# Performance work log

Measured on AMD Instinct MI355X. Metric: run time of the kernel, lower is better.

Reference implementation:

```python
import jax, jax.numpy as jnp
import numpy as np
from jax import lax

B, N, C_PTS = 16, 4096, 64
NPOINT, RADIUS, NSAMPLE = 1024, 0.2, 32
MLP = [64, 64, 128]


def setup_inputs() -> dict:
    key = jax.random.key(0)
    ks = jax.random.split(key, 8)
    inp = {
        "xyz": jax.random.uniform(ks[0], (B, N, 3), jnp.float32),
        "points": jax.random.normal(ks[1], (B, N, C_PTS), jnp.float32),
    }
    cin = C_PTS + 3  # use_xyz=True concatenates centered xyz
    for i, cout in enumerate(MLP):
        inp[f"W{i}"] = jax.random.normal(ks[2 + 2 * i], (cin, cout), jnp.float32) / np.sqrt(cin).astype(np.float32)
        inp[f"b{i}"] = jnp.zeros((cout,), jnp.float32)
        cin = cout
    return inp


def _fps(xyz, npoint):
    # Farthest point sampling (sequential) -> (B, npoint) int32 indices.
    b, n, _ = xyz.shape

    def body(carry, _):
        mind, far = carry  # mind: (B,N) running min sq-dist, far: (B,) current pick
        cen = jnp.take_along_axis(xyz, far[:, None, None], axis=1)  # (B,1,3)
        d = jnp.sum((xyz - cen) ** 2, -1)  # (B,N)
        mind = jnp.minimum(mind, d)
        nxt = jnp.argmax(mind, -1).astype(jnp.int32)
        return (mind, nxt), far

    init = (jnp.full((b, n), 1e10, jnp.float32), jnp.zeros((b,), jnp.int32))
    _, idx = lax.scan(body, init, None, length=npoint)
    return jnp.transpose(idx)  # (B, npoint)


def _ball_query(radius, nsample, xyz, new_xyz):
    # First `nsample` point indices (in original order) within `radius` of each
    # center; short groups padded with the first found index (TF op semantics).
    n = xyz.shape[1]
    d2 = jnp.sum((new_xyz[:, :, None, :] - xyz[:, None, :, :]) ** 2, -1)  # (B,S,N)
    keyv = jnp.where(d2 <= radius * radius, jnp.arange(n, dtype=jnp.int32), n)
    idx = jnp.sort(keyv, axis=-1)[:, :, :nsample]  # smallest indices first
    first = idx[:, :, :1]
    idx = jnp.where(idx == n, first, idx)
    return jnp.minimum(idx, n - 1)


def _group(t, idx):
    # t: (B,N,C), idx: (B,S,K) -> (B,S,K,C)
    return jax.vmap(lambda tb, ib: tb[ib])(t, idx)


def reference(xyz, points, W0, b0, W1, b1, W2, b2):
    fps_idx = _fps(xyz, NPOINT)  # (B,S)
    new_xyz = jnp.take_along_axis(xyz, fps_idx[..., None], axis=1)  # (B,S,3)
    idx = _ball_query(RADIUS, NSAMPLE, xyz, new_xyz)  # (B,S,K)
    grouped_xyz = _group(xyz, idx) - new_xyz[:, :, None, :]  # (B,S,K,3) centered
    grouped_pts = _group(points, idx)  # (B,S,K,C)
    new_points = jnp.concatenate([grouped_xyz, grouped_pts], -1)  # (B,S,K,3+C)
    for W, b in ((W0, b0), (W1, b1), (W2, b2)):  # shared MLP = 1x1 conv + relu
        new_points = jax.nn.relu(jnp.einsum('bskc,cd->bskd', new_points, W) + b)
    new_points = jnp.max(new_points, axis=2)  # max-pool over neighbors -> (B,S,128)
    return new_xyz, new_points, idx
```

## Files before the change

kernel.cpp:

```cpp
#include <hip/hip_runtime.h>

#define NB      16
#define NPTS    4096
#define NPOINT  1024
#define NSAMPLE 32

typedef float v2f __attribute__((ext_vector_type(2)));

__device__ __forceinline__ v2f pk_add(v2f a, v2f b) {
  v2f d;
  asm("v_pk_add_f32 %0, %1, %2" : "=v"(d) : "v"(a), "v"(b));
  return d;
}
__device__ __forceinline__ v2f pk_mul(v2f a, v2f b) {
  v2f d;
  asm("v_pk_mul_f32 %0, %1, %2" : "=v"(d) : "v"(a), "v"(b));
  return d;
}
__device__ __forceinline__ float fnegx(float x) {
  return __int_as_float(__float_as_int(x) ^ 0x80000000);
}

template <int C>
__device__ __forceinline__ int dppi(int v) {
  return __builtin_amdgcn_update_dpp(0, v, C, 0xf, 0xf, true);
}

template <int C>
__device__ __forceinline__ unsigned long long dppmax_u64(unsigned long long k) {
  int lo = dppi<C>((int)(unsigned)k);
  int hi = dppi<C>((int)(k >> 32));
  unsigned long long o = ((unsigned long long)(unsigned)hi << 32) | (unsigned)lo;
  return o > k ? o : k;
}

__device__ __forceinline__ unsigned long long swzmax16_u64(unsigned long long k) {
  int lo = __builtin_amdgcn_ds_swizzle((int)(unsigned)k, 0x401F);
  int hi = __builtin_amdgcn_ds_swizzle((int)(k >> 32), 0x401F);
  unsigned long long o = ((unsigned long long)(unsigned)hi << 32) | (unsigned)lo;
  return o > k ? o : k;
}

union SharedA {
  struct {
    float4 lc4[NPTS];
    float scen[NPOINT * 3];
    unsigned long long part[2][16];
  } f;
  float sw[4096];
};

__global__ __launch_bounds__(512) void fps_p1_kernel(
    const float* __restrict__ xyz, const float* __restrict__ pts,
    const float* __restrict__ W0, float* __restrict__ out_xyz,
    float* __restrict__ P1) {
  __shared__ SharedA sm;
  const int t = threadIdx.x;
  if (blockIdx.x < NB) {
    const int b = blockIdx.x;
    const int lane = t & 63;
    const int wid = t >> 6;
    const float* g = xyz + (size_t)b * NPTS * 3;
    for (int j = t; j < NPTS; j += 512)
      sm.f.lc4[j] = make_float4(g[3 * j], g[3 * j + 1], g[3 * j + 2], 0.0f);
    __syncthreads();
    v2f px2[4], py2[4], pz2[4], mind2[4];
    unsigned nlo[8];
#pragma unroll
    for (int p = 0; p < 4; ++p) {
      const int j0 = t + 512 * (2 * p);
      const float4 a = sm.f.lc4[j0];
      const float4 c = sm.f.lc4[j0 + 512];
      px2[p] = (v2f){a.x, c.x};
      py2[p] = (v2f){a.y, c.y};
      pz2[p] = (v2f){a.z, c.z};
      mind2[p] = (v2f){1e10f, 1e10f};
      nlo[2 * p] = ~(unsigned)j0;
      nlo[2 * p + 1] = ~(unsigned)(j0 + 512);
    }
    float cx, cy, cz;
    {
      const float4 c0 = sm.f.lc4[0];
      cx = c0.x; cy = c0.y; cz = c0.z;
    }
    for (int it = 0; it < NPOINT; ++it) {
      if (t == 0) {
        sm.f.scen[3 * it] = cx; sm.f.scen[3 * it + 1] = cy; sm.f.scen[3 * it + 2] = cz;
      }
      const float ncx = fnegx(cx), ncy = fnegx(cy), ncz = fnegx(cz);
      const v2f ncxx = (v2f){ncx, ncx};
      const v2f ncyy = (v2f){ncy, ncy};
      const v2f nczz = (v2f){ncz, ncz};
#pragma unroll
      for (int p = 0; p < 4; ++p) {
        const v2f dx = pk_add(px2[p], ncxx);
        const v2f dy = pk_add(py2[p], ncyy);
        const v2f dz = pk_add(pz2[p], nczz);
        const v2f xx = pk_mul(dx, dx);
        const v2f yy = pk_mul(dy, dy);
        const v2f zz = pk_mul(dz, dz);
        v2f s = pk_add(xx, yy);
        s = pk_add(s, zz);
        mind2[p].x = fminf(mind2[p].x, s.x);
        mind2[p].y = fminf(mind2[p].y, s.y);
      }
      unsigned long long k[8];
#pragma unroll
      for (int p = 0; p < 4; ++p) {
        k[2 * p] = ((unsigned long long)__float_as_uint(mind2[p].x) << 32) | nlo[2 * p];
        k[2 * p + 1] =
            ((unsigned long long)__float_as_uint(mind2[p].y) << 32) | nlo[2 * p + 1];
      }
#pragma unroll
      for (int s = 4; s; s >>= 1)
#pragma unroll
        for (int i = 0; i < s; ++i) k[i] = k[i] > k[i + s] ? k[i] : k[i + s];
      unsigned long long key = k[0];
      key = dppmax_u64<0xB1>(key);
      key = dppmax_u64<0x4E>(key);
      key = dppmax_u64<0x141>(key);
      key = dppmax_u64<0x140>(key);
      key = swzmax16_u64(key);
      const int buf = it & 1;
      if ((lane & 31) == 0) sm.f.part[buf][wid * 2 + (lane >> 5)] = key;
      __syncthreads();
      unsigned long long rk = sm.f.part[buf][lane & 15];
      rk = dppmax_u64<0xB1>(rk);
      rk = dppmax_u64<0x4E>(rk);
      rk = dppmax_u64<0x141>(rk);
      rk = dppmax_u64<0x140>(rk);
      const unsigned idx = ~(unsigned)rk;
      const float4 c4 = sm.f.lc4[idx];
      cx = c4.x; cy = c4.y; cz = c4.z;
    }
    __syncthreads();
    float* ob = out_xyz + (size_t)b * NPOINT * 3;
    for (int i = t; i < NPOINT * 3; i += 512) ob[i] = sm.f.scen[i];
  } else {
    {
      const float4* w4 = (const float4*)(W0 + 192);
      float4* s4 = (float4*)sm.sw;
#pragma unroll
      for (int m = 0; m < 2; ++m) s4[t + 512 * m] = w4[t + 512 * m];
    }
    __syncthreads();
    const size_t r = (size_t)(blockIdx.x - NB) * 512 + t;
    const float* prow = pts + r * 64;
    float acc[64];
#pragma unroll
    for (int d = 0; d < 64; ++d) acc[d] = 0.0f;
#pragma unroll
    for (int cq = 0; cq < 16; ++cq) {
      const float4 p4 = *(const float4*)(prow + cq * 4);
      const float pv[4] = {p4.x, p4.y, p4.z, p4.w};
#pragma unroll
      for (int u = 0; u < 4; ++u) {
        const int c = cq * 4 + u;
#pragma unroll
        for (int d4 = 0; d4 < 16; ++d4) {
          const float4 w = *(const float4*)(&sm.sw[c * 64 + d4 * 4]);
          acc[d4 * 4 + 0] = fmaf(pv[u], w.x, acc[d4 * 4 + 0]);
          acc[d4 * 4 + 1] = fmaf(pv[u], w.y, acc[d4 * 4 + 1]);
          acc[d4 * 4 + 2] = fmaf(pv[u], w.z, acc[d4 * 4 + 2]);
          acc[d4 * 4 + 3] = fmaf(pv[u], w.w, acc[d4 * 4 + 3]);
        }
      }
    }
    float* o = P1 + r * 64;
#pragma unroll
    for (int d4 = 0; d4 < 16; ++d4)
      *(float4*)(o + d4 * 4) =
          make_float4(acc[d4 * 4], acc[d4 * 4 + 1], acc[d4 * 4 + 2], acc[d4 * 4 + 3]);
  }
}

__global__ __launch_bounds__(256) void ballq_mlp_kernel(
    const float* __restrict__ xyz, const float* __restrict__ new_xyz,
    const float* __restrict__ P1,
    const float* __restrict__ W0, const float* __restrict__ b0,
    const float* __restrict__ W1, const float* __restrict__ b1,
    const float* __restrict__ W2, const float* __restrict__ b2,
    float* __restrict__ out_np, float* __restrict__ out_idx) {
  __shared__ int sidx[8][NSAMPLE];
  const int t = threadIdx.x;
  const int wv = t >> 6, lane = t & 63;
  const int qbase = blockIdx.x * 8;
  const float r2 = (float)(0.2 * 0.2);
  for (int s = 0; s < 2; ++s) {
    const int ql = wv * 2 + s;
    const int q = qbase + ql;
    const int b = q >> 10;
    const float* g = xyz + (size_t)b * NPTS * 3;
    const float nx = new_xyz[(size_t)q * 3];
    const float ny = new_xyz[(size_t)q * 3 + 1];
    const float nz = new_xyz[(size_t)q * 3 + 2];
    int cnt = 0;
    for (int base = 0; base < NPTS; base += 64) {
      const int j = base + lane;
      const float dx = __fsub_rn(g[3 * j], nx);
      const float dy = __fsub_rn(g[3 * j + 1], ny);
      const float dz = __fsub_rn(g[3 * j + 2], nz);
      const float d2 = __fadd_rn(__fadd_rn(__fmul_rn(dx, dx), __fmul_rn(dy, dy)),
                                 __fmul_rn(dz, dz));
      const bool hit = d2 <= r2;
      const unsigned long long m = __ballot(hit);
      const int pos = cnt + __popcll(m & ((1ull << lane) - 1ull));
      if (hit && pos < NSAMPLE) sidx[ql][pos] = j;
      cnt += __popcll(m);
      if (cnt >= NSAMPLE) break;
    }
    const int capped = cnt < NSAMPLE ? cnt : NSAMPLE;
    if (lane < NSAMPLE) {
      const int v = sidx[ql][lane < capped ? lane : 0];
      sidx[ql][lane] = v;
      out_idx[(size_t)q * NSAMPLE + lane] = (float)v;
    }
  }
  __syncthreads();
  const int k = t & 31;
  const int ql = t >> 5;
  const int q = qbase + ql;
  const int b = q >> 10;
  const int idx = sidx[ql][k];
  const float nx = new_xyz[(size_t)q * 3];
  const float ny = new_xyz[(size_t)q * 3 + 1];
  const float nz = new_xyz[(size_t)q * 3 + 2];
  const float* p = xyz + ((size_t)b * NPTS + idx) * 3;
  const float dx = p[0] - nx, dy = p[1] - ny, dz = p[2] - nz;

  float h1[64];
  const float* p1r = P1 + ((size_t)b * NPTS + idx) * 64;
#pragma unroll
  for (int d4 = 0; d4 < 16; ++d4) {
    const float4 pv = *(const float4*)(p1r + d4 * 4);
    const float pe[4] = {pv.x, pv.y, pv.z, pv.w};
#pragma unroll
    for (int u = 0; u < 4; ++u) {
      const int d = d4 * 4 + u;
      const float v = pe[u] + dx * W0[d] + dy * W0[64 + d] + dz * W0[128 + d] + b0[d];
      h1[d] = fmaxf(v, 0.0f);
    }
  }

  float h2[64];
#pragma unroll
  for (int j4 = 0; j4 < 16; ++j4) {
    const float4 bb = *(const float4*)(&b1[j4 * 4]);
    h2[j4 * 4 + 0] = bb.x; h2[j4 * 4 + 1] = bb.y;
    h2[j4 * 4 + 2] = bb.z; h2[j4 * 4 + 3] = bb.w;
  }
#pragma unroll
  for (int c = 0; c < 64; ++c) {
    const float hc = h1[c];
#pragma unroll
    for (int j4 = 0; j4 < 16; ++j4) {
      const float4 w = *(const float4*)(&W1[c * 64 + j4 * 4]);
      h2[j4 * 4 + 0] = fmaf(hc, w.x, h2[j4 * 4 + 0]);
      h2[j4 * 4 + 1] = fmaf(hc, w.y, h2[j4 * 4 + 1]);
      h2[j4 * 4 + 2] = fmaf(hc, w.z, h2[j4 * 4 + 2]);
      h2[j4 * 4 + 3] = fmaf(hc, w.w, h2[j4 * 4 + 3]);
    }
  }
#pragma unroll
  for (int j = 0; j < 64; ++j) h2[j] = fmaxf(h2[j], 0.0f);

  float* outq = out_np + (size_t)q * 128;
  for (int jb = 0; jb < 4; ++jb) {
    float acc[32];
#pragma unroll
    for (int j8 = 0; j8 < 8; ++j8) {
      const float4 bb = *(const float4*)(&b2[jb * 32 + j8 * 4]);
      acc[j8 * 4 + 0] = bb.x; acc[j8 * 4 + 1] = bb.y;
      acc[j8 * 4 + 2] = bb.z; acc[j8 * 4 + 3] = bb.w;
    }
#pragma unroll
    for (int c = 0; c < 64; ++c) {
      const float hc = h2[c];
#pragma unroll
      for (int j8 = 0; j8 < 8; ++j8) {
        const float4 w = *(const float4*)(&W2[c * 128 + jb * 32 + j8 * 4]);
        acc[j8 * 4 + 0] = fmaf(hc, w.x, acc[j8 * 4 + 0]);
        acc[j8 * 4 + 1] = fmaf(hc, w.y, acc[j8 * 4 + 1]);
        acc[j8 * 4 + 2] = fmaf(hc, w.z, acc[j8 * 4 + 2]);
        acc[j8 * 4 + 3] = fmaf(hc, w.w, acc[j8 * 4 + 3]);
      }
    }
#pragma unroll
    for (int j = 0; j < 32; ++j) acc[j] = fmaxf(acc[j], 0.0f);
#pragma unroll
    for (int msk = 16; msk >= 1; msk >>= 1) {
#pragma unroll
      for (int j = 0; j < 32; ++j) acc[j] = fmaxf(acc[j], __shfl_xor(acc[j], msk, 64));
    }
    if (k == 0) {
#pragma unroll
      for (int j8 = 0; j8 < 8; ++j8)
        *(float4*)(outq + jb * 32 + j8 * 4) =
            make_float4(acc[j8 * 4 + 0], acc[j8 * 4 + 1], acc[j8 * 4 + 2], acc[j8 * 4 + 3]);
    }
  }
}

extern "C" void kernel_launch(void* const* d_in, const int* in_sizes, int n_in,
                              void* d_out, int out_size, void* d_ws, size_t ws_size,
                              hipStream_t stream) {
  const float* xyz = (const float*)d_in[0];
  const float* pts = (const float*)d_in[1];
  const float* W0  = (const float*)d_in[2];
  const float* b0  = (const float*)d_in[3];
  const float* W1  = (const float*)d_in[4];
  const float* b1  = (const float*)d_in[5];
  const float* W2  = (const float*)d_in[6];
  const float* b2  = (const float*)d_in[7];

  float* out      = (float*)d_out;
  float* out_xyz  = out;
  float* out_np   = out + 16 * 1024 * 3;
  float* out_idx  = out_np + 16 * 1024 * 128;

  float* P1 = (float*)d_ws;

  fps_p1_kernel<<<NB + 128, 512, 0, stream>>>(xyz, pts, W0, out_xyz, P1);
  ballq_mlp_kernel<<<2048, 256, 0, stream>>>(xyz, out_xyz, P1,
                                             W0, b0, W1, b1, W2, b2,
                                             out_np, out_idx);
}
```

Baseline: 1.006 ms.

## Fuse FPS, projection and ball-query MLP into one cooperative persistent kernel

Merges the two kernels into a single cooperative launch of 256 blocks. Sixteen blocks run farthest-point sampling and publish centroids in chunks of 64 through release flags. The remaining blocks compute the P1 projection, wait on a global counter, then spin on per-chunk flags so ball query and the MLP overlap with the ongoing FPS instead of waiting for it to finish. This removes the serial dependency between sampling and grouping at the cost of spin-wait synchronization, bounded spin loops that could time out and produce wrong results, and a flag memset. It also splits the FPS shared-memory layout into separate x, y and z arrays.

Result: slower. 1.158 ms (+15.1%).

```diff
diff --git a/kernel.cpp b/kernel.cpp
--- a/kernel.cpp
+++ b/kernel.cpp
@@ -4,6 +4,7 @@
 #define NPTS    4096
 #define NPOINT  1024
 #define NSAMPLE 32
+#define NCHUNK  1024
 
 typedef float v2f __attribute__((ext_vector_type(2)));
 
@@ -41,51 +42,57 @@
   return o > k ? o : k;
 }
 
-union SharedA {
+union SharedU {
   struct {
-    float4 lc4[NPTS];
-    float scen[NPOINT * 3];
+    float lx[NPTS], ly[NPTS], lz[NPTS];
     unsigned long long part[2][16];
   } f;
-  float sw[4096];
+  struct {
+    float sw[4096];
+    int sidx[16][NSAMPLE];
+  } c;
+  char pad[82048];
 };
 
-__global__ __launch_bounds__(512) void fps_p1_kernel(
+__global__ __launch_bounds__(512) void mega_kernel(
     const float* __restrict__ xyz, const float* __restrict__ pts,
-    const float* __restrict__ W0, float* __restrict__ out_xyz,
-    float* __restrict__ P1) {
-  __shared__ SharedA sm;
+    const float* __restrict__ W0, const float* __restrict__ b0,
+    const float* __restrict__ W1, const float* __restrict__ b1,
+    const float* __restrict__ W2, const float* __restrict__ b2,
+    float* __restrict__ out_xyz, float* __restrict__ out_np,
+    float* __restrict__ out_idx, float* __restrict__ P1,
+    int* __restrict__ flags, int* __restrict__ p1done) {
+  __shared__ SharedU sm;
   const int t = threadIdx.x;
+  const int wv = t >> 6, lane = t & 63;
+
   if (blockIdx.x < NB) {
     const int b = blockIdx.x;
-    const int lane = t & 63;
-    const int wid = t >> 6;
     const float* g = xyz + (size_t)b * NPTS * 3;
-    for (int j = t; j < NPTS; j += 512)
-      sm.f.lc4[j] = make_float4(g[3 * j], g[3 * j + 1], g[3 * j + 2], 0.0f);
+    for (int j = t; j < NPTS; j += 512) {
+      sm.f.lx[j] = g[3 * j]; sm.f.ly[j] = g[3 * j + 1]; sm.f.lz[j] = g[3 * j + 2];
+    }
     __syncthreads();
     v2f px2[4], py2[4], pz2[4], mind2[4];
     unsigned nlo[8];
 #pragma unroll
     for (int p = 0; p < 4; ++p) {
       const int j0 = t + 512 * (2 * p);
-      const float4 a = sm.f.lc4[j0];
-      const float4 c = sm.f.lc4[j0 + 512];
-      px2[p] = (v2f){a.x, c.x};
-      py2[p] = (v2f){a.y, c.y};
-      pz2[p] = (v2f){a.z, c.z};
+      px2[p] = (v2f){sm.f.lx[j0], sm.f.lx[j0 + 512]};
+      py2[p] = (v2f){sm.f.ly[j0], sm.f.ly[j0 + 512]};
+      pz2[p] = (v2f){sm.f.lz[j0], sm.f.lz[j0 + 512]};
       mind2[p] = (v2f){1e10f, 1e10f};
       nlo[2 * p] = ~(unsigned)j0;
       nlo[2 * p + 1] = ~(unsigned)(j0 + 512);
     }
-    float cx, cy, cz;
-    {
-      const float4 c0 = sm.f.lc4[0];
-      cx = c0.x; cy = c0.y; cz = c0.z;
-    }
+    float cx = sm.f.lx[0], cy = sm.f.ly[0], cz = sm.f.lz[0];
+    float* ob = out_xyz + (size_t)b * NPOINT * 3;
     for (int it = 0; it < NPOINT; ++it) {
       if (t == 0) {
-        sm.f.scen[3 * it] = cx; sm.f.scen[3 * it + 1] = cy; sm.f.scen[3 * it + 2] = cz;
+        ob[3 * it] = cx; ob[3 * it + 1] = cy; ob[3 * it + 2] = cz;
+        if ((it & 63) == 63)
+          __hip_atomic_store(&flags[b * 16 + (it >> 6)], 1, __ATOMIC_RELEASE,
+                             __HIP_MEMORY_SCOPE_AGENT);
       }
       const float ncx = fnegx(cx), ncy = fnegx(cy), ncz = fnegx(cz);
       const v2f ncxx = (v2f){ncx, ncx};
@@ -122,7 +129,7 @@
       key = dppmax_u64<0x140>(key);
       key = swzmax16_u64(key);
       const int buf = it & 1;
-      if ((lane & 31) == 0) sm.f.part[buf][wid * 2 + (lane >> 5)] = key;
+      if ((lane & 31) == 0) sm.f.part[buf][(t >> 6) * 2 + (lane >> 5)] = key;
       __syncthreads();
       unsigned long long rk = sm.f.part[buf][lane & 15];
       rk = dppmax_u64<0xB1>(rk);
@@ -130,173 +137,183 @@
       rk = dppmax_u64<0x141>(rk);
       rk = dppmax_u64<0x140>(rk);
       const unsigned idx = ~(unsigned)rk;
-      const float4 c4 = sm.f.lc4[idx];
-      cx = c4.x; cy = c4.y; cz = c4.z;
-    }
-    __syncthreads();
-    float* ob = out_xyz + (size_t)b * NPOINT * 3;
-    for (int i = t; i < NPOINT * 3; i += 512) ob[i] = sm.f.scen[i];
+      cx = sm.f.lx[idx]; cy = sm.f.ly[idx]; cz = sm.f.lz[idx];
+    }
   } else {
+    const int nb = (int)gridDim.x - NB;
+    const int cb = (int)blockIdx.x - NB;
     {
       const float4* w4 = (const float4*)(W0 + 192);
-      float4* s4 = (float4*)sm.sw;
-#pragma unroll
-      for (int m = 0; m < 2; ++m) s4[t + 512 * m] = w4[t + 512 * m];
+      float4* s4 = (float4*)sm.c.sw;
+      s4[t] = w4[t]; s4[t + 512] = w4[t + 512];
     }
     __syncthreads();
-    const size_t r = (size_t)(blockIdx.x - NB) * 512 + t;
-    const float* prow = pts + r * 64;
-    float acc[64];
-#pragma unroll
-    for (int d = 0; d < 64; ++d) acc[d] = 0.0f;
-#pragma unroll
-    for (int cq = 0; cq < 16; ++cq) {
-      const float4 p4 = *(const float4*)(prow + cq * 4);
-      const float pv[4] = {p4.x, p4.y, p4.z, p4.w};
-#pragma unroll
-      for (int u = 0; u < 4; ++u) {
-        const int c = cq * 4 + u;
-#pragma unroll
-        for (int d4 = 0; d4 < 16; ++d4) {
-          const float4 w = *(const float4*)(&sm.sw[c * 64 + d4 * 4]);
-          acc[d4 * 4 + 0] = fmaf(pv[u], w.x, acc[d4 * 4 + 0]);
-          acc[d4 * 4 + 1] = fmaf(pv[u], w.y, acc[d4 * 4 + 1]);
-          acc[d4 * 4 + 2] = fmaf(pv[u], w.z, acc[d4 * 4 + 2]);
-          acc[d4 * 4 + 3] = fmaf(pv[u], w.w, acc[d4 * 4 + 3]);
-        }
-      }
-    }
-    float* o = P1 + r * 64;
-#pragma unroll
-    for (int d4 = 0; d4 < 16; ++d4)
-      *(float4*)(o + d4 * 4) =
-          make_float4(acc[d4 * 4], acc[d4 * 4 + 1], acc[d4 * 4 + 2], acc[d4 * 4 + 3]);
-  }
-}
-
-__global__ __launch_bounds__(256) void ballq_mlp_kernel(
-    const float* __restrict__ xyz, const float* __restrict__ new_xyz,
-    const float* __restrict__ P1,
-    const float* __restrict__ W0, const float* __restrict__ b0,
-    const float* __restrict__ W1, const float* __restrict__ b1,
-    const float* __restrict__ W2, const float* __restrict__ b2,
-    float* __restrict__ out_np, float* __restrict__ out_idx) {
-  __shared__ int sidx[8][NSAMPLE];
-  const int t = threadIdx.x;
-  const int wv = t >> 6, lane = t & 63;
-  const int qbase = blockIdx.x * 8;
-  const float r2 = (float)(0.2 * 0.2);
-  for (int s = 0; s < 2; ++s) {
-    const int ql = wv * 2 + s;
-    const int q = qbase + ql;
-    const int b = q >> 10;
-    const float* g = xyz + (size_t)b * NPTS * 3;
-    const float nx = new_xyz[(size_t)q * 3];
-    const float ny = new_xyz[(size_t)q * 3 + 1];
-    const float nz = new_xyz[(size_t)q * 3 + 2];
-    int cnt = 0;
-    for (int base = 0; base < NPTS; base += 64) {
-      const int j = base + lane;
-      const float dx = __fsub_rn(g[3 * j], nx);
-      const float dy = __fsub_rn(g[3 * j + 1], ny);
-      const float dz = __fsub_rn(g[3 * j + 2], nz);
-      const float d2 = __fadd_rn(__fadd_rn(__fmul_rn(dx, dx), __fmul_rn(dy, dy)),
-                                 __fmul_rn(dz, dz));
-      const bool hit = d2 <= r2;
-      const unsigned long long m = __ballot(hit);
-      const int pos = cnt + __popcll(m & ((1ull << lane) - 1ull));
-      if (hit && pos < NSAMPLE) sidx[ql][pos] = j;
-      cnt += __popcll(m);
-      if (cnt >= NSAMPLE) break;
-    }
-    const int capped = cnt < NSAMPLE ? cnt : NSAMPLE;
-    if (lane < NSAMPLE) {
-      const int v = sidx[ql][lane < capped ? lane : 0];
-      sidx[ql][lane] = v;
-      out_idx[(size_t)q * NSAMPLE + lane] = (float)v;
-    }
-  }
-  __syncthreads();
-  const int k = t & 31;
-  const int ql = t >> 5;
-  const int q = qbase + ql;
-  const int b = q >> 10;
-  const int idx = sidx[ql][k];
-  const float nx = new_xyz[(size_t)q * 3];
-  const float ny = new_xyz[(size_t)q * 3 + 1];
-  const float nz = new_xyz[(size_t)q * 3 + 2];
-  const float* p = xyz + ((size_t)b * NPTS + idx) * 3;
-  const float dx = p[0] - nx, dy = p[1] - ny, dz = p[2] - nz;
-
-  float h1[64];
-  const float* p1r = P1 + ((size_t)b * NPTS + idx) * 64;
-#pragma unroll
-  for (int d4 = 0; d4 < 16; ++d4) {
-    const float4 pv = *(const float4*)(p1r + d4 * 4);
-    const float pe[4] = {pv.x, pv.y, pv.z, pv.w};
-#pragma unroll
-    for (int u = 0; u < 4; ++u) {
-      const int d = d4 * 4 + u;
-      const float v = pe[u] + dx * W0[d] + dy * W0[64 + d] + dz * W0[128 + d] + b0[d];
-      h1[d] = fmaxf(v, 0.0f);
-    }
-  }
-
-  float h2[64];
-#pragma unroll
-  for (int j4 = 0; j4 < 16; ++j4) {
-    const float4 bb = *(const float4*)(&b1[j4 * 4]);
-    h2[j4 * 4 + 0] = bb.x; h2[j4 * 4 + 1] = bb.y;
-    h2[j4 * 4 + 2] = bb.z; h2[j4 * 4 + 3] = bb.w;
-  }
-#pragma unroll
-  for (int c = 0; c < 64; ++c) {
-    const float hc = h1[c];
-#pragma unroll
-    for (int j4 = 0; j4 < 16; ++j4) {
-      const float4 w = *(const float4*)(&W1[c * 64 + j4 * 4]);
-      h2[j4 * 4 + 0] = fmaf(hc, w.x, h2[j4 * 4 + 0]);
-      h2[j4 * 4 + 1] = fmaf(hc, w.y, h2[j4 * 4 + 1]);
-      h2[j4 * 4 + 2] = fmaf(hc, w.z, h2[j4 * 4 + 2]);
-      h2[j4 * 4 + 3] = fmaf(hc, w.w, h2[j4 * 4 + 3]);
-    }
-  }
-#pragma unroll
-  for (int j = 0; j < 64; ++j) h2[j] = fmaxf(h2[j], 0.0f);
-
-  float* outq = out_np + (size_t)q * 128;
-  for (int jb = 0; jb < 4; ++jb) {
-    float acc[32];
-#pragma unroll
-    for (int j8 = 0; j8 < 8; ++j8) {
-      const float4 bb = *(const float4*)(&b2[jb * 32 + j8 * 4]);
-      acc[j8 * 4 + 0] = bb.x; acc[j8 * 4 + 1] = bb.y;
-      acc[j8 * 4 + 2] = bb.z; acc[j8 * 4 + 3] = bb.w;
-    }
-#pragma unroll
-    for (int c = 0; c < 64; ++c) {
-      const float hc = h2[c];
-#pragma unroll
-      for (int j8 = 0; j8 < 8; ++j8) {
-        const float4 w = *(const float4*)(&W2[c * 128 + jb * 32 + j8 * 4]);
-        acc[j8 * 4 + 0] = fmaf(hc, w.x, acc[j8 * 4 + 0]);
-        acc[j8 * 4 + 1] = fmaf(hc, w.y, acc[j8 * 4 + 1]);
-        acc[j8 * 4 + 2] = fmaf(hc, w.z, acc[j8 * 4 + 2]);
-        acc[j8 * 4 + 3] = fmaf(hc, w.w, acc[j8 * 4 + 3]);
-      }
-    }
-#pragma unroll
-    for (int j = 0; j < 32; ++j) acc[j] = fmaxf(acc[j], 0.0f);
-#pragma unroll
-    for (int msk = 16; msk >= 1; msk >>= 1) {
-#pragma unroll
-      for (int j = 0; j < 32; ++j) acc[j] = fmaxf(acc[j], __shfl_xor(acc[j], msk, 64));
-    }
-    if (k == 0) {
-#pragma unroll
-      for (int j8 = 0; j8 < 8; ++j8)
-        *(float4*)(outq + jb * 32 + j8 * 4) =
-            make_float4(acc[j8 * 4 + 0], acc[j8 * 4 + 1], acc[j8 * 4 + 2], acc[j8 * 4 + 3]);
+    const int rows_per = (NPTS * NB + nb - 1) / nb;
+    const int r0 = cb * rows_per;
+    const int r1 = min(r0 + rows_per, NPTS * NB);
+    for (int r = r0 + t; r < r1; r += 512) {
+      const float* prow = pts + (size_t)r * 64;
+      float acc[64];
+#pragma unroll
+      for (int d = 0; d < 64; ++d) acc[d] = 0.0f;
+#pragma unroll
+      for (int cq = 0; cq < 16; ++cq) {
+        const float4 p4 = *(const float4*)(prow + cq * 4);
+        const float pv[4] = {p4.x, p4.y, p4.z, p4.w};
+#pragma unroll
+        for (int u = 0; u < 4; ++u) {
+          const int cc = cq * 4 + u;
+#pragma unroll
+          for (int d4 = 0; d4 < 16; ++d4) {
+            const float4 w = *(const float4*)(&sm.c.sw[cc * 64 + d4 * 4]);
+            acc[d4 * 4 + 0] = fmaf(pv[u], w.x, acc[d4 * 4 + 0]);
+            acc[d4 * 4 + 1] = fmaf(pv[u], w.y, acc[d4 * 4 + 1]);
+            acc[d4 * 4 + 2] = fmaf(pv[u], w.z, acc[d4 * 4 + 2]);
+            acc[d4 * 4 + 3] = fmaf(pv[u], w.w, acc[d4 * 4 + 3]);
+          }
+        }
+      }
+      float* o = P1 + (size_t)r * 64;
+#pragma unroll
+      for (int d4 = 0; d4 < 16; ++d4)
+        *(float4*)(o + d4 * 4) = make_float4(acc[d4 * 4 + 0], acc[d4 * 4 + 1],
+                                             acc[d4 * 4 + 2], acc[d4 * 4 + 3]);
+    }
+    __syncthreads();
+    if (t == 0) {
+      __threadfence();
+      __hip_atomic_fetch_add(p1done, 1, __ATOMIC_ACQ_REL, __HIP_MEMORY_SCOPE_AGENT);
+    }
+    {
+      int spins = 0;
+      while (__hip_atomic_load(p1done, __ATOMIC_ACQUIRE, __HIP_MEMORY_SCOPE_AGENT) < nb &&
+             ++spins < (1 << 20))
+        __builtin_amdgcn_s_sleep(2);
+    }
+    const float r2 = (float)(0.2 * 0.2);
+    for (int c = cb; c < NCHUNK; c += nb) {
+      const int s16 = c >> 4, b = c & 15;
+      const int q0 = b * NPOINT + s16 * 16;
+      {
+        int spins = 0;
+        while (__hip_atomic_load(&flags[b * 16 + (s16 >> 2)], __ATOMIC_ACQUIRE,
+                                 __HIP_MEMORY_SCOPE_AGENT) == 0 &&
+               ++spins < (1 << 20))
+          __builtin_amdgcn_s_sleep(2);
+      }
+      const float* g = xyz + (size_t)b * NPTS * 3;
+      for (int s = 0; s < 2; ++s) {
+        const int ql = wv * 2 + s;
+        const int q = q0 + ql;
+        const float nx = out_xyz[(size_t)q * 3];
+        const float ny = out_xyz[(size_t)q * 3 + 1];
+        const float nz = out_xyz[(size_t)q * 3 + 2];
+        int cnt = 0;
+        for (int base = 0; base < NPTS; base += 64) {
+          const int j = base + lane;
+          const float dx = __fsub_rn(g[3 * j], nx);
+          const float dy = __fsub_rn(g[3 * j + 1], ny);
+          const float dz = __fsub_rn(g[3 * j + 2], nz);
+          const float d2 = __fadd_rn(__fadd_rn(__fmul_rn(dx, dx), __fmul_rn(dy, dy)),
+                                     __fmul_rn(dz, dz));
+          const bool hit = d2 <= r2;
+          const unsigned long long m = __ballot(hit);
+          const int pos = cnt + __popcll(m & ((1ull << lane) - 1ull));
+          if (hit && pos < NSAMPLE) sm.c.sidx[ql][pos] = j;
+          cnt += __popcll(m);
+          if (cnt >= NSAMPLE) break;
+        }
+        const int capped = cnt < NSAMPLE ? cnt : NSAMPLE;
+        if (lane < NSAMPLE) {
+          const int v = sm.c.sidx[ql][lane < capped ? lane : 0];
+          sm.c.sidx[ql][lane] = v;
+          out_idx[(size_t)q * NSAMPLE + lane] = (float)v;
+        }
+      }
+      __syncthreads();
+      const int k = t & 31;
+      const int ql = t >> 5;
+      const int q = q0 + ql;
+      const int idx = sm.c.sidx[ql][k];
+      const float nx = out_xyz[(size_t)q * 3];
+      const float ny = out_xyz[(size_t)q * 3 + 1];
+      const float nz = out_xyz[(size_t)q * 3 + 2];
+      const float* p = g + (size_t)idx * 3;
+      const float dx = p[0] - nx, dy = p[1] - ny, dz = p[2] - nz;
+
+      float h1[64];
+      const float* p1r = P1 + ((size_t)b * NPTS + idx) * 64;
+#pragma unroll
+      for (int d4 = 0; d4 < 16; ++d4) {
+        const float4 pv = *(const float4*)(p1r + d4 * 4);
+        const float pe[4] = {pv.x, pv.y, pv.z, pv.w};
+#pragma unroll
+        for (int u = 0; u < 4; ++u) {
+          const int d = d4 * 4 + u;
+          const float v = pe[u] + dx * W0[d] + dy * W0[64 + d] + dz * W0[128 + d] + b0[d];
+          h1[d] = fmaxf(v, 0.0f);
+        }
+      }
+      float h2[64];
+#pragma unroll
+      for (int j4 = 0; j4 < 16; ++j4) {
+        const float4 bb = *(const float4*)(&b1[j4 * 4]);
+        h2[j4 * 4 + 0] = bb.x; h2[j4 * 4 + 1] = bb.y;
+        h2[j4 * 4 + 2] = bb.z; h2[j4 * 4 + 3] = bb.w;
+      }
+#pragma unroll
+      for (int cc = 0; cc < 64; ++cc) {
+        const float hc = h1[cc];
+#pragma unroll
+        for (int j4 = 0; j4 < 16; ++j4) {
+          const float4 w = *(const float4*)(&W1[cc * 64 + j4 * 4]);
+          h2[j4 * 4 + 0] = fmaf(hc, w.x, h2[j4 * 4 + 0]);
+          h2[j4 * 4 + 1] = fmaf(hc, w.y, h2[j4 * 4 + 1]);
+          h2[j4 * 4 + 2] = fmaf(hc, w.z, h2[j4 * 4 + 2]);
+          h2[j4 * 4 + 3] = fmaf(hc, w.w, h2[j4 * 4 + 3]);
+        }
+      }
+#pragma unroll
+      for (int j = 0; j < 64; ++j) h2[j] = fmaxf(h2[j], 0.0f);
+
+      float* outq = out_np + (size_t)q * 128;
+      for (int jb = 0; jb < 4; ++jb) {
+        float acc[32];
+#pragma unroll
+        for (int j8 = 0; j8 < 8; ++j8) {
+          const float4 bb = *(const float4*)(&b2[jb * 32 + j8 * 4]);
+          acc[j8 * 4 + 0] = bb.x; acc[j8 * 4 + 1] = bb.y;
+          acc[j8 * 4 + 2] = bb.z; acc[j8 * 4 + 3] = bb.w;
+        }
+#pragma unroll
+        for (int cc = 0; cc < 64; ++cc) {
+          const float hc = h2[cc];
+#pragma unroll
+          for (int j8 = 0; j8 < 8; ++j8) {
+            const float4 w = *(const float4*)(&W2[cc * 128 + jb * 32 + j8 * 4]);
+            acc[j8 * 4 + 0] = fmaf(hc, w.x, acc[j8 * 4 + 0]);
+            acc[j8 * 4 + 1] = fmaf(hc, w.y, acc[j8 * 4 + 1]);
+            acc[j8 * 4 + 2] = fmaf(hc, w.z, acc[j8 * 4 + 2]);
+            acc[j8 * 4 + 3] = fmaf(hc, w.w, acc[j8 * 4 + 3]);
+          }
+        }
+#pragma unroll
+        for (int j = 0; j < 32; ++j) acc[j] = fmaxf(acc[j], 0.0f);
+#pragma unroll
+        for (int msk = 16; msk >= 1; msk >>= 1) {
+#pragma unroll
+          for (int j = 0; j < 32; ++j)
+            acc[j] = fmaxf(acc[j], __shfl_xor(acc[j], msk, 64));
+        }
+        if (k == 0) {
+#pragma unroll
+          for (int j8 = 0; j8 < 8; ++j8)
+            *(float4*)(outq + jb * 32 + j8 * 4) =
+                make_float4(acc[j8 * 4 + 0], acc[j8 * 4 + 1],
+                            acc[j8 * 4 + 2], acc[j8 * 4 + 3]);
+        }
+      }
+      __syncthreads();
     }
   }
 }
@@ -318,10 +335,16 @@
   float* out_np   = out + 16 * 1024 * 3;
   float* out_idx  = out_np + 16 * 1024 * 128;
 
-  float* P1 = (float*)d_ws;
-
-  fps_p1_kernel<<<NB + 128, 512, 0, stream>>>(xyz, pts, W0, out_xyz, P1);
-  ballq_mlp_kernel<<<2048, 256, 0, stream>>>(xyz, out_xyz, P1,
-                                             W0, b0, W1, b1, W2, b2,
-                                             out_np, out_idx);
-}
+  float* P1     = (float*)d_ws;
+  int*   flags  = (int*)((char*)d_ws + (16u << 20));
+  int*   p1done = flags + 256;
+
+  hipMemsetAsync(flags, 0, 2048, stream);
+
+  void* args[] = {(void*)&xyz, (void*)&pts, (void*)&W0, (void*)&b0,
+                  (void*)&W1,  (void*)&b1,  (void*)&W2, (void*)&b2,
+                  (void*)&out_xyz, (void*)&out_np, (void*)&out_idx,
+                  (void*)&P1, (void*)&flags, (void*)&p1done};
+  hipLaunchCooperativeKernel((const void*)mega_kernel, dim3(256), dim3(512),
+                             args, 0, stream);
+}
```

## Split ball query from MLP and stream weights via scalar loads

Applied to the files above, without the earlier changes.

Moves the ball query into its own kernel that writes neighbour indices to workspace, so the MLP kernel no longer waits behind the query and each thread handles one neighbour. Weight and bias reads become explicit s_load_dwordx16 scalar loads into SGPRs, each followed by a wait, replacing per-lane vector loads of uniform data. Layer 3 now works in two 64-wide halves instead of four 32-wide ones. The FPS kernel's shared memory is padded up to about 84 KB, likely to keep other blocks off the CUs running FPS. The costs are an extra launch, an index round trip through global memory, blocking waits after every scalar load, and higher register pressure from the wider accumulators.

New measurement: 1.291 ms. 1.28x slower.

```diff
diff --git a/kernel.cpp b/kernel.cpp
--- a/kernel.cpp
+++ b/kernel.cpp
@@ -5,7 +5,8 @@
 #define NPOINT  1024
 #define NSAMPLE 32
 
-typedef float v2f __attribute__((ext_vector_type(2)));
+typedef float v2f  __attribute__((ext_vector_type(2)));
+typedef float sv16 __attribute__((ext_vector_type(16)));
 
 __device__ __forceinline__ v2f pk_add(v2f a, v2f b) {
   v2f d;
@@ -21,11 +22,25 @@
   return __int_as_float(__float_as_int(x) ^ 0x80000000);
 }
 
+__device__ __forceinline__ void sload16(const float* p, int boff, sv16& a) {
+  asm volatile("s_load_dwordx16 %0, %1, %2\n\t"
+               "s_waitcnt lgkmcnt(0)"
+               : "=&s"(a)
+               : "s"(p), "i"(boff));
+}
+__device__ __forceinline__ void sload32(const float* p, int boff, sv16& a, sv16& b) {
+  asm volatile("s_load_dwordx16 %0, %2, %3\n\t"
+               "s_load_dwordx16 %1, %2, %4\n\t"
+               "s_waitcnt lgkmcnt(0)"
+               : "=&s"(a), "=&s"(b)
+               : "s"(p), "i"(boff), "i"(boff + 64));
+}
+#define EL32(a, b, j) ((j) < 16 ? (a)[(j) & 15] : (b)[(j) & 15])
+
 template <int C>
 __device__ __forceinline__ int dppi(int v) {
   return __builtin_amdgcn_update_dpp(0, v, C, 0xf, 0xf, true);
 }
-
 template <int C>
 __device__ __forceinline__ unsigned long long dppmax_u64(unsigned long long k) {
   int lo = dppi<C>((int)(unsigned)k);
@@ -33,7 +48,6 @@
   unsigned long long o = ((unsigned long long)(unsigned)hi << 32) | (unsigned)lo;
   return o > k ? o : k;
 }
-
 __device__ __forceinline__ unsigned long long swzmax16_u64(unsigned long long k) {
   int lo = __builtin_amdgcn_ds_swizzle((int)(unsigned)k, 0x401F);
   int hi = __builtin_amdgcn_ds_swizzle((int)(k >> 32), 0x401F);
@@ -41,25 +55,25 @@
   return o > k ? o : k;
 }
 
-union SharedA {
+union SharedB {
   struct {
     float4 lc4[NPTS];
     float scen[NPOINT * 3];
     unsigned long long part[2][16];
   } f;
   float sw[4096];
+  char pad[86016];
 };
 
 __global__ __launch_bounds__(512) void fps_p1_kernel(
     const float* __restrict__ xyz, const float* __restrict__ pts,
     const float* __restrict__ W0, float* __restrict__ out_xyz,
     float* __restrict__ P1) {
-  __shared__ SharedA sm;
+  __shared__ SharedB sm;
   const int t = threadIdx.x;
   if (blockIdx.x < NB) {
     const int b = blockIdx.x;
     const int lane = t & 63;
-    const int wid = t >> 6;
     const float* g = xyz + (size_t)b * NPTS * 3;
     for (int j = t; j < NPTS; j += 512)
       sm.f.lc4[j] = make_float4(g[3 * j], g[3 * j + 1], g[3 * j + 2], 0.0f);
@@ -122,7 +136,7 @@
       key = dppmax_u64<0x140>(key);
       key = swzmax16_u64(key);
       const int buf = it & 1;
-      if ((lane & 31) == 0) sm.f.part[buf][wid * 2 + (lane >> 5)] = key;
+      if ((lane & 31) == 0) sm.f.part[buf][(t >> 6) * 2 + (lane >> 5)] = key;
       __syncthreads();
       unsigned long long rk = sm.f.part[buf][lane & 15];
       rk = dppmax_u64<0xB1>(rk);
@@ -140,8 +154,7 @@
     {
       const float4* w4 = (const float4*)(W0 + 192);
       float4* s4 = (float4*)sm.sw;
-#pragma unroll
-      for (int m = 0; m < 2; ++m) s4[t + 512 * m] = w4[t + 512 * m];
+      s4[t] = w4[t]; s4[t + 512] = w4[t + 512];
     }
     __syncthreads();
     const size_t r = (size_t)(blockIdx.x - NB) * 512 + t;
@@ -169,59 +182,61 @@
     float* o = P1 + r * 64;
 #pragma unroll
     for (int d4 = 0; d4 < 16; ++d4)
-      *(float4*)(o + d4 * 4) =
-          make_float4(acc[d4 * 4], acc[d4 * 4 + 1], acc[d4 * 4 + 2], acc[d4 * 4 + 3]);
-  }
-}
-
-__global__ __launch_bounds__(256) void ballq_mlp_kernel(
+      *(float4*)(o + d4 * 4) = make_float4(acc[d4 * 4 + 0], acc[d4 * 4 + 1],
+                                           acc[d4 * 4 + 2], acc[d4 * 4 + 3]);
+  }
+}
+
+__global__ __launch_bounds__(256) void ballq_kernel(const float* __restrict__ xyz,
+                                                    const float* __restrict__ new_xyz,
+                                                    int* __restrict__ ballidx,
+                                                    float* __restrict__ out_idx) {
+  __shared__ int sidx[4][NSAMPLE];
+  const int wv = threadIdx.x >> 6, lane = threadIdx.x & 63;
+  const int q = blockIdx.x * 4 + wv;
+  const int b = q >> 10;
+  const float* g = xyz + (size_t)b * NPTS * 3;
+  const float nx = new_xyz[(size_t)q * 3];
+  const float ny = new_xyz[(size_t)q * 3 + 1];
+  const float nz = new_xyz[(size_t)q * 3 + 2];
+  const float r2 = (float)(0.2 * 0.2);
+  int cnt = 0;
+  for (int base = 0; base < NPTS; base += 64) {
+    const int j = base + lane;
+    const float dx = __fsub_rn(g[3 * j], nx);
+    const float dy = __fsub_rn(g[3 * j + 1], ny);
+    const float dz = __fsub_rn(g[3 * j + 2], nz);
+    const float d2 = __fadd_rn(__fadd_rn(__fmul_rn(dx, dx), __fmul_rn(dy, dy)),
+                               __fmul_rn(dz, dz));
+    const bool hit = d2 <= r2;
+    const unsigned long long m = __ballot(hit);
+    const int pos = cnt + __popcll(m & ((1ull << lane) - 1ull));
+    if (hit && pos < NSAMPLE) sidx[wv][pos] = j;
+    cnt += __popcll(m);
+    if (cnt >= NSAMPLE) break;
+  }
+  __syncthreads();
+  const int capped = cnt < NSAMPLE ? cnt : NSAMPLE;
+  if (lane < NSAMPLE) {
+    const int v = sidx[wv][lane < capped ? lane : 0];
+    ballidx[(size_t)q * NSAMPLE + lane] = v;
+    out_idx[(size_t)q * NSAMPLE + lane] = (float)v;
+  }
+}
+
+__global__ __launch_bounds__(256) void mlp_kernel(
     const float* __restrict__ xyz, const float* __restrict__ new_xyz,
-    const float* __restrict__ P1,
+    const int* __restrict__ ballidx, const float* __restrict__ P1,
     const float* __restrict__ W0, const float* __restrict__ b0,
     const float* __restrict__ W1, const float* __restrict__ b1,
     const float* __restrict__ W2, const float* __restrict__ b2,
-    float* __restrict__ out_np, float* __restrict__ out_idx) {
-  __shared__ int sidx[8][NSAMPLE];
+    float* __restrict__ out_np) {
   const int t = threadIdx.x;
-  const int wv = t >> 6, lane = t & 63;
-  const int qbase = blockIdx.x * 8;
-  const float r2 = (float)(0.2 * 0.2);
-  for (int s = 0; s < 2; ++s) {
-    const int ql = wv * 2 + s;
-    const int q = qbase + ql;
-    const int b = q >> 10;
-    const float* g = xyz + (size_t)b * NPTS * 3;
-    const float nx = new_xyz[(size_t)q * 3];
-    const float ny = new_xyz[(size_t)q * 3 + 1];
-    const float nz = new_xyz[(size_t)q * 3 + 2];
-    int cnt = 0;
-    for (int base = 0; base < NPTS; base += 64) {
-      const int j = base + lane;
-      const float dx = __fsub_rn(g[3 * j], nx);
-      const float dy = __fsub_rn(g[3 * j + 1], ny);
-      const float dz = __fsub_rn(g[3 * j + 2], nz);
-      const float d2 = __fadd_rn(__fadd_rn(__fmul_rn(dx, dx), __fmul_rn(dy, dy)),
-                                 __fmul_rn(dz, dz));
-      const bool hit = d2 <= r2;
-      const unsigned long long m = __ballot(hit);
-      const int pos = cnt + __popcll(m & ((1ull << lane) - 1ull));
-      if (hit && pos < NSAMPLE) sidx[ql][pos] = j;
-      cnt += __popcll(m);
-      if (cnt >= NSAMPLE) break;
-    }
-    const int capped = cnt < NSAMPLE ? cnt : NSAMPLE;
-    if (lane < NSAMPLE) {
-      const int v = sidx[ql][lane < capped ? lane : 0];
-      sidx[ql][lane] = v;
-      out_idx[(size_t)q * NSAMPLE + lane] = (float)v;
-    }
-  }
-  __syncthreads();
-  const int k = t & 31;
-  const int ql = t >> 5;
-  const int q = qbase + ql;
+  const int item = blockIdx.x * 256 + t;
+  const int k = item & 31;
+  const int q = item >> 5;
   const int b = q >> 10;
-  const int idx = sidx[ql][k];
+  const int idx = ballidx[(size_t)q * 32 + k];
   const float nx = new_xyz[(size_t)q * 3];
   const float ny = new_xyz[(size_t)q * 3 + 1];
   const float nz = new_xyz[(size_t)q * 3 + 2];
@@ -231,71 +246,88 @@
   float h1[64];
   const float* p1r = P1 + ((size_t)b * NPTS + idx) * 64;
 #pragma unroll
-  for (int d4 = 0; d4 < 16; ++d4) {
-    const float4 pv = *(const float4*)(p1r + d4 * 4);
-    const float pe[4] = {pv.x, pv.y, pv.z, pv.w};
-#pragma unroll
-    for (int u = 0; u < 4; ++u) {
-      const int d = d4 * 4 + u;
-      const float v = pe[u] + dx * W0[d] + dy * W0[64 + d] + dz * W0[128 + d] + b0[d];
-      h1[d] = fmaxf(v, 0.0f);
+  for (int dq = 0; dq < 4; ++dq) {
+    sv16 wx, wy, wz, bv;
+    sload16(W0, dq * 64, wx);
+    sload16(W0, 256 + dq * 64, wy);
+    sload16(W0, 512 + dq * 64, wz);
+    sload16(b0, dq * 64, bv);
+#pragma unroll
+    for (int u4 = 0; u4 < 4; ++u4) {
+      const float4 pv = *(const float4*)(p1r + dq * 16 + u4 * 4);
+      const float pe[4] = {pv.x, pv.y, pv.z, pv.w};
+#pragma unroll
+      for (int u = 0; u < 4; ++u) {
+        const int e = u4 * 4 + u;
+        const float v = pe[u] + dx * wx[e] + dy * wy[e] + dz * wz[e] + bv[e];
+        h1[dq * 16 + e] = fmaxf(v, 0.0f);
+      }
     }
   }
 
   float h2[64];
-#pragma unroll
-  for (int j4 = 0; j4 < 16; ++j4) {
-    const float4 bb = *(const float4*)(&b1[j4 * 4]);
-    h2[j4 * 4 + 0] = bb.x; h2[j4 * 4 + 1] = bb.y;
-    h2[j4 * 4 + 2] = bb.z; h2[j4 * 4 + 3] = bb.w;
+  {
+    sv16 ba, bb;
+    sload32(b1, 0, ba, bb);
+#pragma unroll
+    for (int j = 0; j < 32; ++j) h2[j] = EL32(ba, bb, j);
+    sv16 bc, bd;
+    sload32(b1, 128, bc, bd);
+#pragma unroll
+    for (int j = 0; j < 32; ++j) h2[32 + j] = EL32(bc, bd, j);
   }
 #pragma unroll
   for (int c = 0; c < 64; ++c) {
     const float hc = h1[c];
-#pragma unroll
-    for (int j4 = 0; j4 < 16; ++j4) {
-      const float4 w = *(const float4*)(&W1[c * 64 + j4 * 4]);
-      h2[j4 * 4 + 0] = fmaf(hc, w.x, h2[j4 * 4 + 0]);
-      h2[j4 * 4 + 1] = fmaf(hc, w.y, h2[j4 * 4 + 1]);
-      h2[j4 * 4 + 2] = fmaf(hc, w.z, h2[j4 * 4 + 2]);
-      h2[j4 * 4 + 3] = fmaf(hc, w.w, h2[j4 * 4 + 3]);
-    }
+    sv16 wa, wb;
+    sload32(W1, c * 256, wa, wb);
+#pragma unroll
+    for (int j = 0; j < 32; ++j) h2[j] = fmaf(hc, EL32(wa, wb, j), h2[j]);
+    sv16 wc, wd;
+    sload32(W1, c * 256 + 128, wc, wd);
+#pragma unroll
+    for (int j = 0; j < 32; ++j) h2[32 + j] = fmaf(hc, EL32(wc, wd, j), h2[32 + j]);
   }
 #pragma unroll
   for (int j = 0; j < 64; ++j) h2[j] = fmaxf(h2[j], 0.0f);
 
   float* outq = out_np + (size_t)q * 128;
-  for (int jb = 0; jb < 4; ++jb) {
-    float acc[32];
-#pragma unroll
-    for (int j8 = 0; j8 < 8; ++j8) {
-      const float4 bb = *(const float4*)(&b2[jb * 32 + j8 * 4]);
-      acc[j8 * 4 + 0] = bb.x; acc[j8 * 4 + 1] = bb.y;
-      acc[j8 * 4 + 2] = bb.z; acc[j8 * 4 + 3] = bb.w;
+#pragma unroll
+  for (int jh = 0; jh < 2; ++jh) {
+    float acc[64];
+    {
+      sv16 ba, bb;
+      sload32(b2, jh * 256, ba, bb);
+#pragma unroll
+      for (int j = 0; j < 32; ++j) acc[j] = EL32(ba, bb, j);
+      sv16 bc, bd;
+      sload32(b2, jh * 256 + 128, bc, bd);
+#pragma unroll
+      for (int j = 0; j < 32; ++j) acc[32 + j] = EL32(bc, bd, j);
     }
 #pragma unroll
     for (int c = 0; c < 64; ++c) {
       const float hc = h2[c];
-#pragma unroll
-      for (int j8 = 0; j8 < 8; ++j8) {
-        const float4 w = *(const float4*)(&W2[c * 128 + jb * 32 + j8 * 4]);
-        acc[j8 * 4 + 0] = fmaf(hc, w.x, acc[j8 * 4 + 0]);
-        acc[j8 * 4 + 1] = fmaf(hc, w.y, acc[j8 * 4 + 1]);
-        acc[j8 * 4 + 2] = fmaf(hc, w.z, acc[j8 * 4 + 2]);
-        acc[j8 * 4 + 3] = fmaf(hc, w.w, acc[j8 * 4 + 3]);
-      }
-    }
-#pragma unroll
-    for (int j = 0; j < 32; ++j) acc[j] = fmaxf(acc[j], 0.0f);
+      sv16 wa, wb;
+      sload32(W2, c * 512 + jh * 256, wa, wb);
+#pragma unroll
+      for (int j = 0; j < 32; ++j) acc[j] = fmaf(hc, EL32(wa, wb, j), acc[j]);
+      sv16 wc, wd;
+      sload32(W2, c * 512 + jh * 256 + 128, wc, wd);
+#pragma unroll
+      for (int j = 0; j < 32; ++j) acc[32 + j] = fmaf(hc, EL32(wc, wd, j), acc[32 + j]);
+    }
+#pragma unroll
+    for (int j = 0; j < 64; ++j) acc[j] = fmaxf(acc[j], 0.0f);
 #pragma unroll
     for (int msk = 16; msk >= 1; msk >>= 1) {
 #pragma unroll
-      for (int j = 0; j < 32; ++j) acc[j] = fmaxf(acc[j], __shfl_xor(acc[j], msk, 64));
+      for (int j = 0; j < 64; ++j) acc[j] = fmaxf(acc[j], __shfl_xor(acc[j], msk, 64));
     }
     if (k == 0) {
 #pragma unroll
-      for (int j8 = 0; j8 < 8; ++j8)
-        *(float4*)(outq + jb * 32 + j8 * 4) =
+      for (int j8 = 0; j8 < 16; ++j8)
+        *(float4*)(outq + jh * 64 + j8 * 4) =
             make_float4(acc[j8 * 4 + 0], acc[j8 * 4 + 1], acc[j8 * 4 + 2], acc[j8 * 4 + 3]);
     }
   }
@@ -318,10 +350,11 @@
   float* out_np   = out + 16 * 1024 * 3;
   float* out_idx  = out_np + 16 * 1024 * 128;
 
-  float* P1 = (float*)d_ws;
+  int*   ballidx = (int*)d_ws;
+  float* P1      = (float*)((char*)d_ws + (2u << 20));
 
   fps_p1_kernel<<<NB + 128, 512, 0, stream>>>(xyz, pts, W0, out_xyz, P1);
-  ballq_mlp_kernel<<<2048, 256, 0, stream>>>(xyz, out_xyz, P1,
-                                             W0, b0, W1, b1, W2, b2,
-                                             out_np, out_idx);
-}
+  ballq_kernel<<<4096, 256, 0, stream>>>(xyz, out_xyz, ballidx, out_idx);
+  mlp_kernel<<<2048, 256, 0, stream>>>(xyz, out_xyz, ballidx, P1,
+                                       W0, b0, W1, b1, W2, b2, out_np);
+}
```
